# Performance work log

Hardware: AMD Instinct MI355X
Metric: run time of the kernel (lower is better)

Reference implementation:

```python
import jax, jax.numpy as jnp
import numpy as np
import math

NUM_HEADS = 8
DIM = 512
SEQ = 128
LAG = 5
DH = DIM // NUM_HEADS


def setup_inputs() -> dict:
    key = jax.random.key(0)
    ks = jax.random.split(key, 10)
    b = 64
    scale = 0.02
    inp = {
        "input": jax.random.normal(ks[0], (b, LAG, SEQ, DIM), dtype=jnp.float32),
        "Wq": jax.random.normal(ks[1], (DIM, DIM), dtype=jnp.float32) * scale,
        "bq": jnp.zeros((DIM,), dtype=jnp.float32),
        "Wk": jax.random.normal(ks[2], (DIM, DIM), dtype=jnp.float32) * scale,
        "bk": jnp.zeros((DIM,), dtype=jnp.float32),
        "Wv": jax.random.normal(ks[3], (DIM, DIM), dtype=jnp.float32) * scale,
        "bv": jnp.zeros((DIM,), dtype=jnp.float32),
        "Wo": jax.random.normal(ks[4], (LAG * DIM, DIM), dtype=jnp.float32) * scale,
        "bo": jnp.zeros((DIM,), dtype=jnp.float32),
    }
    return inp


def reference(input, Wq, bq, Wk, bk, Wv, bv, Wo, bo):
    b, l, s, dim = input.shape
    h, Dh = NUM_HEADS, DH
    last = input[:, -1]                                   # (b, s, dim) -- q/v only use final lag
    # projections -> split heads
    q = (last @ Wq + bq).reshape(b, s, h, Dh).transpose(0, 2, 1, 3)       # (b, h, s, Dh)
    v = (last @ Wv + bv).reshape(b, s, h, Dh).transpose(0, 2, 1, 3)       # (b, h, s, Dh)
    k = (input @ Wk + bk).reshape(b, l, s, h, Dh).transpose(0, 1, 3, 2, 4)  # (b, l, h, s, Dh)
    # q broadcast across the lag dim
    scores = jnp.einsum('bhid,blhjd->blhij', q, k) / math.sqrt(Dh)        # (b, l, h, s, s)
    causal = jnp.tril(jnp.ones((s, s), dtype=bool))
    scores = jnp.where(causal, scores, -jnp.inf)
    # original subtracts max then calls softmax; mathematically identical to stable softmax
    weights = jax.nn.softmax(scores, axis=-1)                             # (b, l, h, s, s)
    inter = jnp.einsum('blhij,bhjd->blhid', weights, v)                   # (b, l, h, s, Dh)
    # rearrange 'b l h s d -> b s (l h d)'
    inter = inter.transpose(0, 3, 1, 2, 4).reshape(b, s, l * h * Dh)
    return inter @ Wo + bo                                                # (b, s, dim)
```

## Files before the change

kernel.cpp:

```cpp
#include <hip/hip_runtime.h>
#include <math.h>

#define NHEADS 8
#define DIMC   512
#define SEQC   128
#define LAGC   5
#define DHC    64
#define BATCHC 64

typedef __attribute__((ext_vector_type(8))) short short8;
typedef __attribute__((ext_vector_type(4))) float f32x4;
typedef __attribute__((ext_vector_type(8))) unsigned short ushort8;

__device__ inline unsigned short f2b(float f) {
    unsigned int x = __float_as_uint(f);
    x += 0x7fffu + ((x >> 16) & 1u);
    return (unsigned short)(x >> 16);
}
__device__ inline float b2f(unsigned short u) {
    return __uint_as_float((unsigned)u << 16);
}

__device__ inline void load_lds16(const void* g, void* l) {
    __builtin_amdgcn_global_load_lds(
        (const __attribute__((address_space(1))) void*)g,
        (__attribute__((address_space(3))) void*)l, 16, 0, 0);
}

__global__ __launch_bounds__(256)
void f32_to_bf16_kernel(const float* __restrict__ in, unsigned short* __restrict__ out,
                        long long n8)
{
    for (long long i = (long long)blockIdx.x * blockDim.x + threadIdx.x; i < n8;
         i += (long long)gridDim.x * blockDim.x) {
        const float4 a = *(const float4*)(in + i * 8);
        const float4 b = *(const float4*)(in + i * 8 + 4);
        uint4 u;
        u.x = (unsigned)f2b(a.x) | ((unsigned)f2b(a.y) << 16);
        u.y = (unsigned)f2b(a.z) | ((unsigned)f2b(a.w) << 16);
        u.z = (unsigned)f2b(b.x) | ((unsigned)f2b(b.y) << 16);
        u.w = (unsigned)f2b(b.z) | ((unsigned)f2b(b.w) << 16);
        *(uint4*)(out + i * 8) = u;
    }
}

__global__ __launch_bounds__(256)
void transpose_bf16_kernel(const float* __restrict__ W, unsigned short* __restrict__ Wt,
                           int K, int N)
{
    __shared__ float t[32][33];
    const int k0 = blockIdx.x * 32, n0 = blockIdx.y * 32;
    const int tx = threadIdx.x & 31, ty = threadIdx.x >> 5;
    #pragma unroll
    for (int i = 0; i < 32; i += 8)
        t[ty + i][tx] = W[(long long)(k0 + ty + i) * N + n0 + tx];
    __syncthreads();
    #pragma unroll
    for (int i = 0; i < 32; i += 8)
        Wt[(long long)(n0 + ty + i) * K + k0 + tx] = f2b(t[tx][ty + i]);
}

template<bool BF16OUT>
__global__ __launch_bounds__(256)
void gemm_mfma(const unsigned short* __restrict__ A, const unsigned short* __restrict__ Bt,
               const float* __restrict__ bias1, const float* __restrict__ bias2, int nsplit,
               void* __restrict__ Cv, int N, int K, int lda, int group, long long gstride)
{
    __shared__ __align__(16) unsigned short As[128][32];
    __shared__ __align__(16) unsigned short Bs[128][32];

    const int tid  = threadIdx.x;
    const int w    = tid >> 6;
    const int lane = tid & 63;
    const int bm = blockIdx.y * 128;
    const int bn = blockIdx.x * 128;
    const int wr = (w >> 1) * 64;
    const int wc = (w & 1) * 64;

    const int srow   = w * 32 + (lane >> 2);
    const int schunk = (lane & 3) * 8;
    const int am0 = bm + srow;
    const int am1 = am0 + 16;
    const unsigned short* ag0 = A + (long long)(am0 / group) * gstride
                                  + (long long)(am0 % group) * lda + schunk;
    const unsigned short* ag1 = A + (long long)(am1 / group) * gstride
                                  + (long long)(am1 % group) * lda + schunk;
    const unsigned short* bg0 = Bt + (long long)(bn + srow) * K + schunk;
    const unsigned short* bg1 = bg0 + (long long)16 * K;
    unsigned short* lA0 = &As[w * 32][0];
    unsigned short* lA1 = &As[w * 32 + 16][0];
    unsigned short* lB0 = &Bs[w * 32][0];
    unsigned short* lB1 = &Bs[w * 32 + 16][0];

    const int n  = lane & 15;
    const int g8 = (lane >> 4) * 8;

    f32x4 acc[4][4];
    #pragma unroll
    for (int i = 0; i < 4; ++i)
        #pragma unroll
        for (int j = 0; j < 4; ++j) acc[i][j] = (f32x4){0.f, 0.f, 0.f, 0.f};

    for (int k0 = 0; k0 < K; k0 += 32) {
        load_lds16(ag0, lA0);
        load_lds16(ag1, lA1);
        load_lds16(bg0, lB0);
        load_lds16(bg1, lB1);
        ag0 += 32; ag1 += 32; bg0 += 32; bg1 += 32;
        __syncthreads();

        short8 af[4], bf[4];
        #pragma unroll
        for (int t = 0; t < 4; ++t) {
            af[t] = *(const short8*)&As[wr + t * 16 + n][g8];
            bf[t] = *(const short8*)&Bs[wc + t * 16 + n][g8];
        }
        #pragma unroll
        for (int i = 0; i < 4; ++i)
            #pragma unroll
            for (int j = 0; j < 4; ++j)
                acc[i][j] = __builtin_amdgcn_mfma_f32_16x16x32_bf16(
                    af[i], bf[j], acc[i][j], 0, 0, 0);
        __syncthreads();
    }

    const bool second = (bn >= nsplit);
    const float* bp = second ? bias2 : bias1;
    const int boff = second ? nsplit : 0;
    const int crow0 = bm + wr + (lane >> 4) * 4;
    const int ccol0 = bn + wc + n;
    float bvals[4];
    #pragma unroll
    for (int j = 0; j < 4; ++j) bvals[j] = bp[ccol0 + j * 16 - boff];
    #pragma unroll
    for (int i = 0; i < 4; ++i)
        #pragma unroll
        for (int j = 0; j < 4; ++j) {
            const int col = ccol0 + j * 16;
            #pragma unroll
            for (int r = 0; r < 4; ++r) {
                const float v = acc[i][j][r] + bvals[j];
                const long long idx = (long long)(crow0 + i * 16 + r) * N + col;
                if (BF16OUT) ((unsigned short*)Cv)[idx] = f2b(v);
                else         ((float*)Cv)[idx] = v;
            }
        }
}

__global__ __launch_bounds__(256)
void attn_mfma_kernel(const unsigned short* __restrict__ QV,
                      const unsigned short* __restrict__ Kp,
                      unsigned short* __restrict__ inter)
{
    __shared__ __align__(16) unsigned short PK[128 * 136];
    __shared__ __align__(16) unsigned short Vt[64 * 136];

    const int bid = blockIdx.x;
    const int h = bid & 7;
    const int b = bid >> 3;
    const int tid = threadIdx.x;
    const int w = tid >> 6, lane = tid & 63;
    const int n = lane & 15, g = lane >> 4;
    const int g8 = g * 8;
    const int wr = w * 32;

    {
        const int j = tid >> 1, d0 = (tid & 1) * 32;
        const unsigned short* vsrc = QV + ((long long)(b * SEQC + j)) * (2 * DIMC)
                                        + DIMC + h * DHC + d0;
        ushort8 vv[4];
        #pragma unroll
        for (int c = 0; c < 4; ++c) vv[c] = *(const ushort8*)(vsrc + c * 8);
        #pragma unroll
        for (int c = 0; c < 4; ++c)
            #pragma unroll
            for (int e = 0; e < 8; ++e)
                Vt[(d0 + c * 8 + e) * 136 + j] = vv[c][e];
    }

    short8 qf[2][2];
    #pragma unroll
    for (int rb = 0; rb < 2; ++rb)
        #pragma unroll
        for (int ks = 0; ks < 2; ++ks)
            qf[rb][ks] = *(const short8*)(QV + ((long long)(b * SEQC + wr + rb * 16 + n)) * (2 * DIMC)
                                             + h * DHC + ks * 32 + g8);

    const int jrow = tid >> 1, jc = (tid & 1) * 32;
    const unsigned short* ksrc = Kp + ((long long)((b * LAGC) * SEQC + jrow)) * DIMC
                                    + h * DHC + jc;
    ushort8 kreg[4];
    #pragma unroll
    for (int c = 0; c < 4; ++c) kreg[c] = *(const ushort8*)(ksrc + c * 8);

    const int cbm0 = (2 * w + 0) | 1;
    const int cbm1 = (2 * w + 1) | 1;
    const int nk0 = (cbm0 + 1) >> 1;
    const int nk1 = (cbm1 + 1) >> 1;

    for (int l = 0; l < LAGC; ++l) {
        __syncthreads();
        #pragma unroll
        for (int c = 0; c < 4; ++c)
            *(ushort8*)&PK[jrow * 72 + jc + c * 8] = kreg[c];
        __syncthreads();

        f32x4 accs[2][8];
        #pragma unroll
        for (int cb = 0; cb < 8; ++cb) {
            if (cb <= cbm1) {
                const short8 bf0 = *(const short8*)&PK[(cb * 16 + n) * 72 + g8];
                const short8 bf1 = *(const short8*)&PK[(cb * 16 + n) * 72 + 32 + g8];
                if (cb <= cbm0) {
                    accs[0][cb] = (f32x4){0.f, 0.f, 0.f, 0.f};
                    accs[0][cb] = __builtin_amdgcn_mfma_f32_16x16x32_bf16(qf[0][0], bf0, accs[0][cb], 0, 0, 0);
                    accs[0][cb] = __builtin_amdgcn_mfma_f32_16x16x32_bf16(qf[0][1], bf1, accs[0][cb], 0, 0, 0);
                }
                accs[1][cb] = (f32x4){0.f, 0.f, 0.f, 0.f};
                accs[1][cb] = __builtin_amdgcn_mfma_f32_16x16x32_bf16(qf[1][0], bf0, accs[1][cb], 0, 0, 0);
                accs[1][cb] = __builtin_amdgcn_mfma_f32_16x16x32_bf16(qf[1][1], bf1, accs[1][cb], 0, 0, 0);
            }
        }
        __syncthreads();

        if (l + 1 < LAGC) {
            const unsigned short* knext = ksrc + (long long)(l + 1) * SEQC * DIMC;
            #pragma unroll
            for (int c = 0; c < 4; ++c) kreg[c] = *(const ushort8*)(knext + c * 8);
        }

        float inv[2][4];
        #pragma unroll
        for (int rb = 0; rb < 2; ++rb) {
            const int cbm = rb ? cbm1 : cbm0;
            float ps[4] = {0.f, 0.f, 0.f, 0.f};
            #pragma unroll
            for (int cb = 0; cb < 8; ++cb) {
                if (cb <= cbm) {
                    const int j = cb * 16 + n;
                    #pragma unroll
                    for (int r = 0; r < 4; ++r) {
                        const int qr = wr + rb * 16 + 4 * g + r;
                        float p = __builtin_exp2f(accs[rb][cb][r] * 0.18033688f);
                        p = (j <= qr) ? p : 0.f;
                        ps[r] += p;
                        PK[qr * 136 + j] = f2b(p);
                    }
                }
            }
            #pragma unroll
            for (int r = 0; r < 4; ++r) {
                float s = ps[r];
                s += __shfl_xor(s, 1, 64);
                s += __shfl_xor(s, 2, 64);
                s += __shfl_xor(s, 4, 64);
                s += __shfl_xor(s, 8, 64);
                inv[rb][r] = 1.f / s;
            }
        }

        asm volatile("s_waitcnt lgkmcnt(0)" ::: "memory");

        f32x4 acco[2][4];
        #pragma unroll
        for (int rb = 0; rb < 2; ++rb)
            #pragma unroll
            for (int db = 0; db < 4; ++db) acco[rb][db] = (f32x4){0.f, 0.f, 0.f, 0.f};
        #pragma unroll
        for (int ks2 = 0; ks2 < 4; ++ks2) {
            if (ks2 < nk1) {
                short8 bv[4];
                #pragma unroll
                for (int db = 0; db < 4; ++db)
                    bv[db] = *(const short8*)&Vt[(db * 16 + n) * 136 + ks2 * 32 + g8];
                const short8 pa1 = *(const short8*)&PK[(wr + 16 + n) * 136 + ks2 * 32 + g8];
                if (ks2 < nk0) {
                    const short8 pa0 = *(const short8*)&PK[(wr + n) * 136 + ks2 * 32 + g8];
                    #pragma unroll
                    for (int db = 0; db < 4; ++db)
                        acco[0][db] = __builtin_amdgcn_mfma_f32_16x16x32_bf16(pa0, bv[db], acco[0][db], 0, 0, 0);
                }
                #pragma unroll
                for (int db = 0; db < 4; ++db)
                    acco[1][db] = __builtin_amdgcn_mfma_f32_16x16x32_bf16(pa1, bv[db], acco[1][db], 0, 0, 0);
            }
        }

        unsigned short* obase = inter + (long long)(b * SEQC) * (LAGC * DIMC)
                                      + l * DIMC + h * DHC;
        #pragma unroll
        for (int rb = 0; rb < 2; ++rb)
            #pragma unroll
            for (int db = 0; db < 4; ++db)
                #pragma unroll
                for (int r = 0; r < 4; ++r) {
                    const int qr = wr + rb * 16 + 4 * g + r;
                    obase[(long long)qr * (LAGC * DIMC) + db * 16 + n] =
                        f2b(acco[rb][db][r] * inv[rb][r]);
                }
    }
}

extern "C" void kernel_launch(void* const* d_in, const int* in_sizes, int n_in,
                              void* d_out, int out_size, void* d_ws, size_t ws_size,
                              hipStream_t stream)
{
    const float* input = (const float*)d_in[0];
    const float* Wq = (const float*)d_in[1];
    const float* bq = (const float*)d_in[2];
    const float* Wk = (const float*)d_in[3];
    const float* bk = (const float*)d_in[4];
    const float* Wv = (const float*)d_in[5];
    const float* bv = (const float*)d_in[6];
    const float* Wo = (const float*)d_in[7];
    const float* bo = (const float*)d_in[8];
    float* out = (float*)d_out;

    const long long MQ = (long long)BATCHC * SEQC;
    const long long MK = (long long)BATCHC * LAGC * SEQC;
    const int BIG = 1 << 30;

    unsigned short* in_bf = (unsigned short*)d_ws;
    unsigned short* Wqvt  = in_bf + MK * DIMC;
    unsigned short* Wkt   = Wqvt + (long long)2 * DIMC * DIMC;
    unsigned short* Wot   = Wkt + (long long)DIMC * DIMC;
    unsigned short* QV    = Wot + (long long)DIMC * (LAGC * DIMC);
    unsigned short* Kb    = QV + MQ * (2 * DIMC);
    unsigned short* inter = Kb + MK * DIMC;

    f32_to_bf16_kernel<<<2048, 256, 0, stream>>>(input, in_bf, MK * DIMC / 8);
    transpose_bf16_kernel<<<dim3(DIMC / 32, DIMC / 32), 256, 0, stream>>>(Wq, Wqvt, DIMC, DIMC);
    transpose_bf16_kernel<<<dim3(DIMC / 32, DIMC / 32), 256, 0, stream>>>(
        Wv, Wqvt + (long long)DIMC * DIMC, DIMC, DIMC);
    transpose_bf16_kernel<<<dim3(DIMC / 32, DIMC / 32), 256, 0, stream>>>(Wk, Wkt, DIMC, DIMC);
    transpose_bf16_kernel<<<dim3(LAGC * DIMC / 32, DIMC / 32), 256, 0, stream>>>(
        Wo, Wot, LAGC * DIMC, DIMC);

    const long long bstride = (long long)LAGC * SEQC * DIMC;
    const unsigned short* last_bf = in_bf + (long long)(LAGC - 1) * SEQC * DIMC;

    gemm_mfma<true><<<dim3(2 * DIMC / 128, MQ / 128), 256, 0, stream>>>(
        last_bf, Wqvt, bq, bv, DIMC, QV, 2 * DIMC, DIMC, DIMC, SEQC, bstride);
    gemm_mfma<true><<<dim3(DIMC / 128, MK / 128), 256, 0, stream>>>(
        in_bf, Wkt, bk, bk, BIG, Kb, DIMC, DIMC, DIMC, BIG, 0);

    attn_mfma_kernel<<<dim3(BATCHC * NHEADS), 256, 0, stream>>>(QV, Kb, inter);

    gemm_mfma<false><<<dim3(DIMC / 128, MQ / 128), 256, 0, stream>>>(
        inter, Wot, bo, bo, BIG, out, DIMC, LAGC * DIMC, LAGC * DIMC, BIG, 0);
}
```

Before: 335.4 us.

## Add triple-buffered LDS pipeline to K and output GEMMs, merge weight transposes

Introduces a gemm_pipe kernel with three LDS stages. Async global-to-LDS loads for tile t+2 are issued while tile t is computed, using vmcnt waits and one barrier per iteration instead of two. The K projection and output projection GEMMs switch to it, while the QV GEMM keeps the original kernel. The four weight transpose launches are folded into one 3D launch to cut launch overhead. This adds LDS usage per block, which may lower occupancy.

```diff
diff --git a/kernel.cpp b/kernel.cpp
--- a/kernel.cpp
+++ b/kernel.cpp
@@ -45,11 +45,21 @@
 }
 
 __global__ __launch_bounds__(256)
-void transpose_bf16_kernel(const float* __restrict__ W, unsigned short* __restrict__ Wt,
-                           int K, int N)
-{
+void transpose4_bf16_kernel(const float* __restrict__ Wq, const float* __restrict__ Wv,
+                            const float* __restrict__ Wk, const float* __restrict__ Wo,
+                            unsigned short* __restrict__ Tq, unsigned short* __restrict__ Tv,
+                            unsigned short* __restrict__ Tk, unsigned short* __restrict__ To)
+{
+    const int z = blockIdx.z;
+    const int K = (z == 3) ? LAGC * DIMC : DIMC;
+    const int k0 = blockIdx.x * 32;
+    if (k0 >= K) return;
+    const float* W = (z == 0) ? Wq : (z == 1) ? Wv : (z == 2) ? Wk : Wo;
+    unsigned short* Wt = (z == 0) ? Tq : (z == 1) ? Tv : (z == 2) ? Tk : To;
+    const int N = DIMC;
+    const int n0 = blockIdx.y * 32;
+
     __shared__ float t[32][33];
-    const int k0 = blockIdx.x * 32, n0 = blockIdx.y * 32;
     const int tx = threadIdx.x & 31, ty = threadIdx.x >> 5;
     #pragma unroll
     for (int i = 0; i < 32; i += 8)
@@ -62,7 +72,7 @@
 
 template<bool BF16OUT>
 __global__ __launch_bounds__(256)
-void gemm_mfma(const unsigned short* __restrict__ A, const unsigned short* __restrict__ Bt,
+void gemm_base(const unsigned short* __restrict__ A, const unsigned short* __restrict__ Bt,
                const float* __restrict__ bias1, const float* __restrict__ bias2, int nsplit,
                void* __restrict__ Cv, int N, int K, int lda, int group, long long gstride)
 {
@@ -122,6 +132,108 @@
                 acc[i][j] = __builtin_amdgcn_mfma_f32_16x16x32_bf16(
                     af[i], bf[j], acc[i][j], 0, 0, 0);
         __syncthreads();
+    }
+
+    const bool second = (bn >= nsplit);
+    const float* bp = second ? bias2 : bias1;
+    const int boff = second ? nsplit : 0;
+    const int crow0 = bm + wr + (lane >> 4) * 4;
+    const int ccol0 = bn + wc + n;
+    float bvals[4];
+    #pragma unroll
+    for (int j = 0; j < 4; ++j) bvals[j] = bp[ccol0 + j * 16 - boff];
+    #pragma unroll
+    for (int i = 0; i < 4; ++i)
+        #pragma unroll
+        for (int j = 0; j < 4; ++j) {
+            const int col = ccol0 + j * 16;
+            #pragma unroll
+            for (int r = 0; r < 4; ++r) {
+                const float v = acc[i][j][r] + bvals[j];
+                const long long idx = (long long)(crow0 + i * 16 + r) * N + col;
+                if (BF16OUT) ((unsigned short*)Cv)[idx] = f2b(v);
+                else         ((float*)Cv)[idx] = v;
+            }
+        }
+}
+
+template<bool BF16OUT>
+__global__ __launch_bounds__(256)
+void gemm_pipe(const unsigned short* __restrict__ A, const unsigned short* __restrict__ Bt,
+               const float* __restrict__ bias1, const float* __restrict__ bias2, int nsplit,
+               void* __restrict__ Cv, int N, int K, int lda, int group, long long gstride)
+{
+    __shared__ __align__(16) unsigned short As[3][128][32];
+    __shared__ __align__(16) unsigned short Bs[3][128][32];
+
+    const int tid  = threadIdx.x;
+    const int w    = tid >> 6;
+    const int lane = tid & 63;
+    const int bm = blockIdx.y * 128;
+    const int bn = blockIdx.x * 128;
+    const int wr = (w >> 1) * 64;
+    const int wc = (w & 1) * 64;
+
+    const int srow   = w * 32 + (lane >> 2);
+    const int schunk = (lane & 3) * 8;
+    const int am0 = bm + srow;
+    const int am1 = am0 + 16;
+    const unsigned short* ag0 = A + (long long)(am0 / group) * gstride
+                                  + (long long)(am0 % group) * lda + schunk;
+    const unsigned short* ag1 = A + (long long)(am1 / group) * gstride
+                                  + (long long)(am1 % group) * lda + schunk;
+    const unsigned short* bg0 = Bt + (long long)(bn + srow) * K + schunk;
+    const unsigned short* bg1 = bg0 + (long long)16 * K;
+
+    const int n  = lane & 15;
+    const int g8 = (lane >> 4) * 8;
+
+    const int nt = K >> 5;
+
+    load_lds16(ag0, &As[0][w * 32][0]);
+    load_lds16(ag1, &As[0][w * 32 + 16][0]);
+    load_lds16(bg0, &Bs[0][w * 32][0]);
+    load_lds16(bg1, &Bs[0][w * 32 + 16][0]);
+    load_lds16(ag0 + 32, &As[1][w * 32][0]);
+    load_lds16(ag1 + 32, &As[1][w * 32 + 16][0]);
+    load_lds16(bg0 + 32, &Bs[1][w * 32][0]);
+    load_lds16(bg1 + 32, &Bs[1][w * 32 + 16][0]);
+
+    f32x4 acc[4][4];
+    #pragma unroll
+    for (int i = 0; i < 4; ++i)
+        #pragma unroll
+        for (int j = 0; j < 4; ++j) acc[i][j] = (f32x4){0.f, 0.f, 0.f, 0.f};
+
+    int cur = 0;
+    for (int t = 0; t < nt; ++t) {
+        if (t == nt - 1) asm volatile("s_waitcnt vmcnt(0)" ::: "memory");
+        else             asm volatile("s_waitcnt vmcnt(4)" ::: "memory");
+        __builtin_amdgcn_s_barrier();
+
+        if (t + 2 < nt) {
+            const int b2 = cur + 2 >= 3 ? cur - 1 : cur + 2;
+            const int ko = (t + 2) << 5;
+            load_lds16(ag0 + ko, &As[b2][w * 32][0]);
+            load_lds16(ag1 + ko, &As[b2][w * 32 + 16][0]);
+            load_lds16(bg0 + ko, &Bs[b2][w * 32][0]);
+            load_lds16(bg1 + ko, &Bs[b2][w * 32 + 16][0]);
+        }
+
+        short8 af[4], bf[4];
+        #pragma unroll
+        for (int tt = 0; tt < 4; ++tt) {
+            af[tt] = *(const short8*)&As[cur][wr + tt * 16 + n][g8];
+            bf[tt] = *(const short8*)&Bs[cur][wc + tt * 16 + n][g8];
+        }
+        #pragma unroll
+        for (int i = 0; i < 4; ++i)
+            #pragma unroll
+            for (int j = 0; j < 4; ++j)
+                acc[i][j] = __builtin_amdgcn_mfma_f32_16x16x32_bf16(
+                    af[i], bf[j], acc[i][j], 0, 0, 0);
+
+        cur = cur + 1 >= 3 ? 0 : cur + 1;
     }
 
     const bool second = (bn >= nsplit);
@@ -329,23 +441,20 @@
     unsigned short* inter = Kb + MK * DIMC;
 
     f32_to_bf16_kernel<<<2048, 256, 0, stream>>>(input, in_bf, MK * DIMC / 8);
-    transpose_bf16_kernel<<<dim3(DIMC / 32, DIMC / 32), 256, 0, stream>>>(Wq, Wqvt, DIMC, DIMC);
-    transpose_bf16_kernel<<<dim3(DIMC / 32, DIMC / 32), 256, 0, stream>>>(
-        Wv, Wqvt + (long long)DIMC * DIMC, DIMC, DIMC);
-    transpose_bf16_kernel<<<dim3(DIMC / 32, DIMC / 32), 256, 0, stream>>>(Wk, Wkt, DIMC, DIMC);
-    transpose_bf16_kernel<<<dim3(LAGC * DIMC / 32, DIMC / 32), 256, 0, stream>>>(
-        Wo, Wot, LAGC * DIMC, DIMC);
+    transpose4_bf16_kernel<<<dim3(LAGC * DIMC / 32, DIMC / 32, 4), 256, 0, stream>>>(
+        Wq, Wv, Wk, Wo,
+        Wqvt, Wqvt + (long long)DIMC * DIMC, Wkt, Wot);
 
     const long long bstride = (long long)LAGC * SEQC * DIMC;
     const unsigned short* last_bf = in_bf + (long long)(LAGC - 1) * SEQC * DIMC;
 
-    gemm_mfma<true><<<dim3(2 * DIMC / 128, MQ / 128), 256, 0, stream>>>(
+    gemm_base<true><<<dim3(2 * DIMC / 128, MQ / 128), 256, 0, stream>>>(
         last_bf, Wqvt, bq, bv, DIMC, QV, 2 * DIMC, DIMC, DIMC, SEQC, bstride);
-    gemm_mfma<true><<<dim3(DIMC / 128, MK / 128), 256, 0, stream>>>(
+    gemm_pipe<true><<<dim3(DIMC / 128, MK / 128), 256, 0, stream>>>(
         in_bf, Wkt, bk, bk, BIG, Kb, DIMC, DIMC, DIMC, BIG, 0);
 
     attn_mfma_kernel<<<dim3(BATCHC * NHEADS), 256, 0, stream>>>(QV, Kb, inter);
 
-    gemm_mfma<false><<<dim3(DIMC / 128, MQ / 128), 256, 0, stream>>>(
+    gemm_pipe<false><<<dim3(DIMC / 128, MQ / 128), 256, 0, stream>>>(
         inter, Wot, bo, bo, BIG, out, DIMC, LAGC * DIMC, LAGC * DIMC, BIG, 0);
 }
```

Result: faster. 315.9 us (-5.8%).
